# Performance work log

Measured on AMD Instinct MI355X. Metric: run time of the kernel, lower is better.

Reference implementation:

```python
import jax, jax.numpy as jnp
import numpy as np
import math

VOCAB = 128000
D_MODEL = 1024
CUTOFFS = [20000, 60000, VOCAB]  # cluster boundaries (last = vocab_size)
B, S = 8, 4096


def setup_inputs() -> dict:
    key = jax.random.key(0)
    ks = jax.random.split(key, 6)
    input_ids = jax.random.randint(ks[0], (B, S), 0, VOCAB)
    # cluster 0: ids [0, 20000), dim 1024, padding_idx=0 -> zero row
    emb0 = jax.random.normal(ks[1], (20000, 1024), jnp.float32)
    emb0 = emb0.at[0].set(0.0)
    # cluster 1: ids [20000, 60000), dim 256 (= 1024 // 4**1)
    emb1 = jax.random.normal(ks[2], (40000, 256), jnp.float32)
    # cluster 2: ids [60000, 128000), dim 64 (= 1024 // 4**2)
    emb2 = jax.random.normal(ks[3], (68000, 64), jnp.float32)
    # nn.Linear(emb_dim, d_model, bias=False): weight shape [d_model, emb_dim]
    proj1 = jax.random.normal(ks[4], (1024, 256), jnp.float32) * 0.02
    proj2 = jax.random.normal(ks[5], (1024, 64), jnp.float32) * 0.02
    return {"input_ids": input_ids, "emb0": emb0, "emb1": emb1, "emb2": emb2,
            "proj1": proj1, "proj2": proj2}


def reference(input_ids, emb0, emb1, emb2, proj1, proj2):
    d_model = emb0.shape[1]
    starts = [0, CUTOFFS[0], CUTOFFS[1]]
    ends = CUTOFFS
    tables = [emb0, emb1, emb2]
    projs = [None, proj1, proj2]
    out = jnp.zeros(input_ids.shape + (d_model,), jnp.float32)
    for start, end, tab, proj in zip(starts, ends, tables, projs):
        mask = (input_ids >= start) & (input_ids < end)          # [B,S]
        local = jnp.clip(input_ids - start, 0, tab.shape[0] - 1)  # in-range gather ids
        e = tab[local]                                            # [B,S,emb_dim]
        if proj is not None:
            e = jnp.einsum('bse,de->bsd', e, proj)                # project to d_model
        else:
            # padding_idx=0: row is zero; mask keeps grad out of row 0 too
            e = e * (input_ids != 0)[..., None].astype(e.dtype)
        out = out + jnp.where(mask[..., None], e, 0.0)            # masked scatter
    return out * math.sqrt(d_model)
```

## Files before the change

kernel.cpp:

```cpp
#include <hip/hip_runtime.h>
#include <hip/hip_bf16.h>


typedef __attribute__((ext_vector_type(4))) float        float4v;
typedef __attribute__((ext_vector_type(8))) short        short8;
typedef __attribute__((ext_vector_type(2))) unsigned int uint2v;

#define D_MODEL 1024

__device__ __forceinline__ short f2bf(float x) {
    unsigned u = __builtin_bit_cast(unsigned, x);
    unsigned r = u + 0x7fffu + ((u >> 16) & 1u);
    return (short)(r >> 16);
}

__device__ __forceinline__ short8 cvt8(float4v a, float4v b) {
    short8 r;
    r[0] = f2bf(a[0]); r[1] = f2bf(a[1]); r[2] = f2bf(a[2]); r[3] = f2bf(a[3]);
    r[4] = f2bf(b[0]); r[5] = f2bf(b[1]); r[6] = f2bf(b[2]); r[7] = f2bf(b[3]);
    return r;
}

__device__ __forceinline__ uint2v pack4(float4v v) {
    uint2v r;
    r[0] = (unsigned)(unsigned short)f2bf(v[0]) | ((unsigned)(unsigned short)f2bf(v[1]) << 16);
    r[1] = (unsigned)(unsigned short)f2bf(v[2]) | ((unsigned)(unsigned short)f2bf(v[3]) << 16);
    return r;
}

__global__ __launch_bounds__(256)
void prep_k(const int* __restrict__ ids, int n, int pb,
            int* __restrict__ cnt,
            int* __restrict__ l0, int* __restrict__ l1, int* __restrict__ l2,
            const float* __restrict__ proj1, const float* __restrict__ proj2,
            uint2v* __restrict__ p1bf, uint2v* __restrict__ p2bf)
{
    const int b = blockIdx.x;
    if (b >= pb) {
        if (b < pb + 256) {
            int t = (b - pb) * 256 + threadIdx.x;
            p1bf[t] = pack4(((const float4v*)proj1)[t]);
        } else {
            int t = (b - pb - 256) * 256 + threadIdx.x;
            p2bf[t] = pack4(((const float4v*)proj2)[t]);
        }
        return;
    }
    int i = b * blockDim.x + threadIdx.x;
    int lane = threadIdx.x & 63;
    int id = (i < n) ? ids[i] : -1;
    bool is0 = (i < n) && (id < 20000);
    bool is1 = (i < n) && (id >= 20000) && (id < 60000);
    bool is2 = (i < n) && (id >= 60000);
    unsigned long long ltmask = (lane == 0) ? 0ull : (~0ull >> (64 - lane));

    unsigned long long m;
    m = __ballot(is0);
    if (m) {
        int leader = __ffsll(m) - 1;
        int base = 0;
        if (lane == leader) base = atomicAdd(&cnt[2], __popcll(m));
        base = __shfl(base, leader);
        if (is0) l0[base + __popcll(m & ltmask)] = i;
    }
    m = __ballot(is1);
    if (m) {
        int leader = __ffsll(m) - 1;
        int base = 0;
        if (lane == leader) base = atomicAdd(&cnt[0], __popcll(m));
        base = __shfl(base, leader);
        if (is1) l1[base + __popcll(m & ltmask)] = i;
    }
    m = __ballot(is2);
    if (m) {
        int leader = __ffsll(m) - 1;
        int base = 0;
        if (lane == leader) base = atomicAdd(&cnt[1], __popcll(m));
        base = __shfl(base, leader);
        if (is2) l2[base + __popcll(m & ltmask)] = i;
    }
}

__global__ __launch_bounds__(256)
void copy_c0(const int* __restrict__ ids, const int* __restrict__ l0,
             const int* __restrict__ cnt,
             const float* __restrict__ emb0, float* __restrict__ out)
{
    const int count0 = cnt[2];
    for (int b = blockIdx.x; b < count0; b += gridDim.x) {
        int t = l0[b];
        int id = ids[t];
        const float4v* src = (const float4v*)(emb0 + (size_t)id * D_MODEL);
        float4v*       dst = (float4v*)(out + (size_t)t * D_MODEL);
        dst[threadIdx.x] = src[threadIdx.x] * 32.0f;
    }
}

template<int K, int START>
__global__ __launch_bounds__(512)
void gemm_proj(const int* __restrict__ ids,
               const float* __restrict__ table,
               const short* __restrict__ pbf,
               const int* __restrict__ list,
               const int* __restrict__ cnt_ptr,
               float* __restrict__ out)
{
    const int count  = *cnt_ptr;
    const int m_base = blockIdx.x * 32;
    if (m_base >= count) return;

    __shared__ int s_tok[32];
    __shared__ int s_loc[32];
    const int tid = threadIdx.x;
    if (tid < 32) {
        int m   = m_base + tid;
        int tok = (m < count) ? list[m] : -1;
        s_tok[tid] = tok;
        s_loc[tid] = (tok >= 0) ? (ids[tok] - START) : 0;
    }
    __syncthreads();

    const int lane = tid & 63;
    const int wave = tid >> 6;
    const int col  = lane & 15;
    const int quad = lane >> 4;

    const float* arow0 = table + (size_t)s_loc[col]      * K + quad * 8;
    const float* arow1 = table + (size_t)s_loc[16 + col] * K + quad * 8;
    const short* bbase = pbf   + (size_t)(wave * 128 + col) * K + quad * 8;

    float4v acc0[8], acc1[8];
#pragma unroll
    for (int i = 0; i < 8; i++) {
        acc0[i] = (float4v){0.f, 0.f, 0.f, 0.f};
        acc1[i] = (float4v){0.f, 0.f, 0.f, 0.f};
    }

#pragma unroll
    for (int ks = 0; ks < K; ks += 32) {
        short8 a0 = cvt8(*(const float4v*)(arow0 + ks),
                         *(const float4v*)(arow0 + ks + 4));
        short8 a1 = cvt8(*(const float4v*)(arow1 + ks),
                         *(const float4v*)(arow1 + ks + 4));
#pragma unroll
        for (int nt = 0; nt < 8; nt++) {
            short8 b = *(const short8*)(bbase + (size_t)nt * 16 * K + ks);
            acc0[nt] = __builtin_amdgcn_mfma_f32_16x16x32_bf16(a0, b, acc0[nt], 0, 0, 0);
            acc1[nt] = __builtin_amdgcn_mfma_f32_16x16x32_bf16(a1, b, acc1[nt], 0, 0, 0);
        }
    }

#pragma unroll
    for (int r = 0; r < 4; r++) {
        int row = quad * 4 + r;
        if (m_base + row < count) {
            float* orow = out + (size_t)s_tok[row] * D_MODEL + wave * 128 + col;
#pragma unroll
            for (int nt = 0; nt < 8; nt++) orow[nt * 16] = acc0[nt][r] * 32.0f;
        }
        if (m_base + 16 + row < count) {
            float* orow = out + (size_t)s_tok[16 + row] * D_MODEL + wave * 128 + col;
#pragma unroll
            for (int nt = 0; nt < 8; nt++) orow[nt * 16] = acc1[nt][r] * 32.0f;
        }
    }
}

extern "C" void kernel_launch(void* const* d_in, const int* in_sizes, int n_in,
                              void* d_out, int out_size, void* d_ws, size_t ws_size,
                              hipStream_t stream)
{
    const int*   ids   = (const int*)  d_in[0];
    const float* emb0  = (const float*)d_in[1];
    const float* emb1  = (const float*)d_in[2];
    const float* emb2  = (const float*)d_in[3];
    const float* proj1 = (const float*)d_in[4];
    const float* proj2 = (const float*)d_in[5];
    float*       out   = (float*)d_out;
    const int n = in_sizes[0];

    int*   cnt  = (int*)d_ws;
    int*   l0   = (int*)((char*)d_ws + 256);
    int*   l1   = l0 + n;
    int*   l2   = l1 + n;
    size_t poff = (256 + (size_t)3 * n * 4 + 255) & ~(size_t)255;
    short* p1bf = (short*)((char*)d_ws + poff);
    short* p2bf = p1bf + 1024 * 256;

    const int pb = (n + 255) / 256;

    hipMemsetAsync(cnt, 0, 4 * sizeof(int), stream);
    prep_k<<<pb + 256 + 64, 256, 0, stream>>>(ids, n, pb, cnt, l0, l1, l2,
                                              proj1, proj2,
                                              (uint2v*)p1bf, (uint2v*)p2bf);
    copy_c0<<<2048, 256, 0, stream>>>(ids, l0, cnt, emb0, out);
    gemm_proj<256, 20000><<<(n + 31) / 32, 512, 0, stream>>>(ids, emb1, p1bf, l1, &cnt[0], out);
    gemm_proj< 64, 60000><<<(n + 31) / 32, 512, 0, stream>>>(ids, emb2, p2bf, l2, &cnt[1], out);
}
```

Measured before the change: 308.2 us.

## Fuse cluster copy and projection GEMMs into one persistent work-queue kernel

Replaces the three separate launches (cluster-0 copy and two projection GEMMs) with a single persistent kernel of 2048 blocks. Each block walks a unified work range covering GEMM tiles for cluster 1, then cluster 2, then paired cluster-0 row copies. This removes two launch boundaries and the tail idle time between kernels, and lets copy work overlap GEMM work. In exchange it adds a __syncthreads per GEMM tile for shared-memory reuse, and all work types now run at the 512-thread launch bounds, which may limit register budget or occupancy for the copy path.

```diff
diff --git a/kernel.cpp b/kernel.cpp
--- a/kernel.cpp
+++ b/kernel.cpp
@@ -81,36 +81,18 @@
     }
 }
 
-__global__ __launch_bounds__(256)
-void copy_c0(const int* __restrict__ ids, const int* __restrict__ l0,
-             const int* __restrict__ cnt,
-             const float* __restrict__ emb0, float* __restrict__ out)
-{
-    const int count0 = cnt[2];
-    for (int b = blockIdx.x; b < count0; b += gridDim.x) {
-        int t = l0[b];
-        int id = ids[t];
-        const float4v* src = (const float4v*)(emb0 + (size_t)id * D_MODEL);
-        float4v*       dst = (float4v*)(out + (size_t)t * D_MODEL);
-        dst[threadIdx.x] = src[threadIdx.x] * 32.0f;
-    }
-}
-
 template<int K, int START>
-__global__ __launch_bounds__(512)
-void gemm_proj(const int* __restrict__ ids,
+__device__ __forceinline__
+void gemm_tile(int tile,
+               const int* __restrict__ ids,
                const float* __restrict__ table,
                const short* __restrict__ pbf,
                const int* __restrict__ list,
-               const int* __restrict__ cnt_ptr,
-               float* __restrict__ out)
-{
-    const int count  = *cnt_ptr;
-    const int m_base = blockIdx.x * 32;
-    if (m_base >= count) return;
-
-    __shared__ int s_tok[32];
-    __shared__ int s_loc[32];
+               int count,
+               float* __restrict__ out,
+               int* s_tok, int* s_loc)
+{
+    const int m_base = tile * 32;
     const int tid = threadIdx.x;
     if (tid < 32) {
         int m   = m_base + tid;
@@ -162,6 +144,58 @@
             float* orow = out + (size_t)s_tok[16 + row] * D_MODEL + wave * 128 + col;
 #pragma unroll
             for (int nt = 0; nt < 8; nt++) orow[nt * 16] = acc1[nt][r] * 32.0f;
+        }
+    }
+    __syncthreads();
+}
+
+__device__ __forceinline__
+void copy_item(int item, const int* __restrict__ ids,
+               const int* __restrict__ l0, int count0,
+               const float* __restrict__ emb0, float* __restrict__ out)
+{
+    int r = item * 2 + (threadIdx.x >> 8);
+    if (r < count0) {
+        int t  = l0[r];
+        int id = ids[t];
+        const float4v* src = (const float4v*)(emb0 + (size_t)id * D_MODEL);
+        float4v*       dst = (float4v*)(out + (size_t)t * D_MODEL);
+        int c = threadIdx.x & 255;
+        dst[c] = src[c] * 32.0f;
+    }
+}
+
+__global__ __launch_bounds__(512)
+void fused_main(const int* __restrict__ ids,
+                const float* __restrict__ emb0,
+                const float* __restrict__ emb1,
+                const float* __restrict__ emb2,
+                const short* __restrict__ p1bf,
+                const short* __restrict__ p2bf,
+                const int* __restrict__ l0,
+                const int* __restrict__ l1,
+                const int* __restrict__ l2,
+                const int* __restrict__ cnt,
+                float* __restrict__ out)
+{
+    __shared__ int s_tok[32];
+    __shared__ int s_loc[32];
+
+    const int c1 = cnt[0];
+    const int c2 = cnt[1];
+    const int c0 = cnt[2];
+    const int t1 = (c1 + 31) >> 5;
+    const int t2 = (c2 + 31) >> 5;
+    const int tc = (c0 + 1) >> 1;
+    const int total = t1 + t2 + tc;
+
+    for (int w = blockIdx.x; w < total; w += gridDim.x) {
+        if (w < t1) {
+            gemm_tile<256, 20000>(w, ids, emb1, p1bf, l1, c1, out, s_tok, s_loc);
+        } else if (w < t1 + t2) {
+            gemm_tile<64, 60000>(w - t1, ids, emb2, p2bf, l2, c2, out, s_tok, s_loc);
+        } else {
+            copy_item(w - t1 - t2, ids, l0, c0, emb0, out);
         }
     }
 }
@@ -193,7 +227,6 @@
     prep_k<<<pb + 256 + 64, 256, 0, stream>>>(ids, n, pb, cnt, l0, l1, l2,
                                               proj1, proj2,
                                               (uint2v*)p1bf, (uint2v*)p2bf);
-    copy_c0<<<2048, 256, 0, stream>>>(ids, l0, cnt, emb0, out);
-    gemm_proj<256, 20000><<<(n + 31) / 32, 512, 0, stream>>>(ids, emb1, p1bf, l1, &cnt[0], out);
-    gemm_proj< 64, 60000><<<(n + 31) / 32, 512, 0, stream>>>(ids, emb2, p2bf, l2, &cnt[1], out);
-}
+    fused_main<<<2048, 512, 0, stream>>>(ids, emb0, emb1, emb2,
+                                         p1bf, p2bf, l0, l1, l2, cnt, out);
+}
```

New measurement: 305.6 us. About the same (-0.8%).
